# Kernel optimization log

Measured on AMD Instinct MI355X. Metric: run time of the kernel, lower is better.

## Reference

```python
import jax, jax.numpy as jnp
import numpy as np


def sh_enc_deg4(d):
    # d: [N,3] in [0,1]; tcnn maps to [-1,1] then evaluates degree-4 real SH (16 coeffs)
    v = d * 2.0 - 1.0
    x, y, z = v[:, 0], v[:, 1], v[:, 2]
    xy, yz, xz = x * y, y * z, x * z
    x2, y2, z2 = x * x, y * y, z * z
    sh = jnp.stack([
        jnp.full_like(x, 0.28209479177387814),
        -0.48860251190291987 * y,
        0.48860251190291987 * z,
        -0.48860251190291987 * x,
        1.0925484305920792 * xy,
        -1.0925484305920792 * yz,
        0.94617469575755997 * z2 - 0.31539156525251999,
        -1.0925484305920792 * xz,
        0.54627421529603959 * (x2 - y2),
        0.59004358992664352 * y * (-3.0 * x2 + y2),
        2.8906114426405538 * xy * z,
        0.45704579946446572 * y * (1.0 - 5.0 * z2),
        0.3731763325901154 * z * (5.0 * z2 - 3.0),
        0.45704579946446572 * x * (1.0 - 5.0 * z2),
        1.4453057213202769 * z * (x2 - y2),
        0.59004358992664352 * x * (x2 - 3.0 * y2),
    ], axis=-1)  # [N,16]
    return sh


def setup_inputs() -> dict:
    key = jax.random.key(0)
    k1, k2, k3, k4 = jax.random.split(key, 4)
    N = 2_097_152
    x = jax.random.uniform(k1, (N, 19), dtype=jnp.float32)
    # bias-free FullyFusedMLP: 32 -> 64 -> 64 -> 3
    W1 = jax.random.normal(k2, (32, 64), dtype=jnp.float32) * (1.0 / np.sqrt(32))
    W2 = jax.random.normal(k3, (64, 64), dtype=jnp.float32) * (1.0 / np.sqrt(64))
    W3 = jax.random.normal(k4, (64, 3), dtype=jnp.float32) * (1.0 / np.sqrt(64))
    return {"x": x, "W1": W1, "W2": W2, "W3": W3}


def reference(x, W1, W2, W3):
    # Composite encoding: SH(deg 4) on first 3 dims, Identity on the other 16 -> 32 features
    enc = jnp.concatenate([sh_enc_deg4(x[:, :3]), x[:, 3:]], axis=-1)  # [N,32]
    h = jax.nn.relu(enc @ W1)   # [N,64]
    h = jax.nn.relu(h @ W2)     # [N,64]
    out = h @ W3                # [N,3], linear output
    return out
```

## Files before the change

### kernel.cpp

```cpp
#include <hip/hip_runtime.h>
#include <hip/hip_bf16.h>


typedef short short8 __attribute__((ext_vector_type(8)));
typedef short short4v __attribute__((ext_vector_type(4)));
typedef float f32x4 __attribute__((ext_vector_type(4)));

#define MFMA16(a, b, c) __builtin_amdgcn_mfma_f32_16x16x32_bf16((a), (b), (c), 0, 0, 0)

static __device__ __forceinline__ short f2bf(float f) {
  __hip_bfloat16 h = __float2bfloat16(f);
  return __builtin_bit_cast(short, h);
}

#define LDS_PAD 68

__global__ __launch_bounds__(256) void fused_color_mlp(
    const float* __restrict__ x, const float* __restrict__ W1,
    const float* __restrict__ W2, const float* __restrict__ W3,
    float* __restrict__ out, int N) {
  __shared__ short h1s[4][16][LDS_PAD];
  __shared__ short h2s[4][16][LDS_PAD];

  const int tid = threadIdx.x;
  const int wv = tid >> 6;
  const int lane = tid & 63;
  const int row = lane & 15;
  const int kg = lane >> 4;

  short8 w1b[4];
#pragma unroll
  for (int cb = 0; cb < 4; ++cb) {
    short8 t;
#pragma unroll
    for (int j = 0; j < 8; ++j) t[j] = f2bf(W1[(kg * 8 + j) * 64 + cb * 16 + row]);
    w1b[cb] = t;
  }
  short8 w2b[2][4];
#pragma unroll
  for (int s = 0; s < 2; ++s)
#pragma unroll
    for (int cb = 0; cb < 4; ++cb) {
      short8 t;
#pragma unroll
      for (int j = 0; j < 8; ++j)
        t[j] = f2bf(W2[(s * 32 + kg * 8 + j) * 64 + cb * 16 + row]);
      w2b[s][cb] = t;
    }
  short8 w3b[2];
  const int c3r = (row < 3) ? row : 2;
#pragma unroll
  for (int s = 0; s < 2; ++s) {
    short8 t;
#pragma unroll
    for (int j = 0; j < 8; ++j) {
      short w = f2bf(W3[(s * 32 + kg * 8 + j) * 3 + c3r]);
      t[j] = (row < 3) ? w : (short)0;
    }
    w3b[s] = t;
  }

  const f32x4 zero = {0.f, 0.f, 0.f, 0.f};
  const long long gw = (long long)blockIdx.x * 4 + wv;
  const long long base = gw * 256;

  for (int it = 0; it < 16; ++it) {
    const long long p0 = base + (long long)it * 16;
    long long p = p0 + row;
    if (p > (long long)N - 1) p = (long long)N - 1;

    const float* xr = x + p * 19;
    const int off = (kg < 2) ? 0 : (3 + (kg - 2) * 8);
    float v[8];
#pragma unroll
    for (int j = 0; j < 8; ++j) v[j] = xr[off + j];

    float e[8];
    if (kg == 0) {
      float X = v[0] * 2.f - 1.f, Y = v[1] * 2.f - 1.f, Z = v[2] * 2.f - 1.f;
      e[0] = 0.28209479177387814f;
      e[1] = -0.48860251190291987f * Y;
      e[2] = 0.48860251190291987f * Z;
      e[3] = -0.48860251190291987f * X;
      e[4] = 1.0925484305920792f * X * Y;
      e[5] = -1.0925484305920792f * Y * Z;
      e[6] = 0.94617469575756f * Z * Z - 0.31539156525252f;
      e[7] = -1.0925484305920792f * X * Z;
    } else if (kg == 1) {
      float X = v[0] * 2.f - 1.f, Y = v[1] * 2.f - 1.f, Z = v[2] * 2.f - 1.f;
      float X2 = X * X, Y2 = Y * Y, Z2 = Z * Z;
      e[0] = 0.5462742152960396f * (X2 - Y2);
      e[1] = 0.5900435899266435f * Y * (-3.f * X2 + Y2);
      e[2] = 2.890611442640554f * X * Y * Z;
      e[3] = 0.4570457994644657f * Y * (1.f - 5.f * Z2);
      e[4] = 0.3731763325901154f * Z * (5.f * Z2 - 3.f);
      e[5] = 0.4570457994644657f * X * (1.f - 5.f * Z2);
      e[6] = 1.445305721320277f * Z * (X2 - Y2);
      e[7] = 0.5900435899266435f * X * (X2 - 3.f * Y2);
    } else {
#pragma unroll
      for (int j = 0; j < 8; ++j) e[j] = v[j];
    }
    short8 a0;
#pragma unroll
    for (int j = 0; j < 8; ++j) a0[j] = f2bf(e[j]);

    f32x4 c1[4];
#pragma unroll
    for (int cb = 0; cb < 4; ++cb) c1[cb] = MFMA16(a0, w1b[cb], zero);

#pragma unroll
    for (int cb = 0; cb < 4; ++cb)
#pragma unroll
      for (int r = 0; r < 4; ++r)
        h1s[wv][kg * 4 + r][cb * 16 + row] = f2bf(fmaxf(c1[cb][r], 0.f));
    __syncthreads();

    short8 a1[2];
#pragma unroll
    for (int s = 0; s < 2; ++s) {
      short4v lo = *(const short4v*)&h1s[wv][row][s * 32 + kg * 8];
      short4v hi = *(const short4v*)&h1s[wv][row][s * 32 + kg * 8 + 4];
      a1[s] = __builtin_shufflevector(lo, hi, 0, 1, 2, 3, 4, 5, 6, 7);
    }

    f32x4 c2[4];
#pragma unroll
    for (int cb = 0; cb < 4; ++cb) {
      f32x4 acc = MFMA16(a1[0], w2b[0][cb], zero);
      c2[cb] = MFMA16(a1[1], w2b[1][cb], acc);
    }

#pragma unroll
    for (int cb = 0; cb < 4; ++cb)
#pragma unroll
      for (int r = 0; r < 4; ++r)
        h2s[wv][kg * 4 + r][cb * 16 + row] = f2bf(fmaxf(c2[cb][r], 0.f));
    __syncthreads();

    short8 a2[2];
#pragma unroll
    for (int s = 0; s < 2; ++s) {
      short4v lo = *(const short4v*)&h2s[wv][row][s * 32 + kg * 8];
      short4v hi = *(const short4v*)&h2s[wv][row][s * 32 + kg * 8 + 4];
      a2[s] = __builtin_shufflevector(lo, hi, 0, 1, 2, 3, 4, 5, 6, 7);
    }

    f32x4 c3 = MFMA16(a2[0], w3b[0], zero);
    c3 = MFMA16(a2[1], w3b[1], c3);

    if (row < 3) {
#pragma unroll
      for (int r = 0; r < 4; ++r) {
        const long long q = p0 + kg * 4 + r;
        if (q < N) out[q * 3 + row] = c3[r];
      }
    }
  }
}

extern "C" void kernel_launch(void* const* d_in, const int* in_sizes, int n_in,
                              void* d_out, int out_size, void* d_ws, size_t ws_size,
                              hipStream_t stream) {
  (void)d_ws; (void)ws_size; (void)n_in; (void)out_size;
  const float* x = (const float*)d_in[0];
  const float* W1 = (const float*)d_in[1];
  const float* W2 = (const float*)d_in[2];
  const float* W3 = (const float*)d_in[3];
  float* out = (float*)d_out;
  const int N = in_sizes[0] / 19;
  const int blocks = (N + 1023) / 1024;
  fused_color_mlp<<<blocks, 256, 0, stream>>>(x, W1, W2, W3, out, N);
}
```

Baseline: 273.4 us.

## Move W3 fragments to LDS, raise occupancy bound, use 32-bit indexing

Stores the padded W3 bf16 fragments in shared memory and reloads them each iteration through an opaque pointer, so they no longer occupy registers for the whole kernel. Adds a min-blocks hint of 8 to launch_bounds so the compiler caps register use for higher occupancy. Replaces 64-bit index math with 32-bit ints to cut scalar and vector address work. The cost is extra LDS reads every iteration, one extra block barrier, and possible register spilling under the tighter bound.

```diff
diff --git a/kernel.cpp b/kernel.cpp
--- a/kernel.cpp
+++ b/kernel.cpp
@@ -14,19 +14,32 @@
 }
 
 #define LDS_PAD 68
+#define ITERS 16
 
-__global__ __launch_bounds__(256) void fused_color_mlp(
+__global__ __launch_bounds__(256, 8) void fused_color_mlp(
     const float* __restrict__ x, const float* __restrict__ W1,
     const float* __restrict__ W2, const float* __restrict__ W3,
     float* __restrict__ out, int N) {
   __shared__ short h1s[4][16][LDS_PAD];
   __shared__ short h2s[4][16][LDS_PAD];
+  __shared__ short w3f[64][16];
 
   const int tid = threadIdx.x;
   const int wv = tid >> 6;
   const int lane = tid & 63;
   const int row = lane & 15;
   const int kg = lane >> 4;
+
+  if (tid < 64) {
+    const int c3r = (row < 3) ? row : 2;
+#pragma unroll
+    for (int s = 0; s < 2; ++s)
+#pragma unroll
+      for (int j = 0; j < 8; ++j) {
+        short w = f2bf(W3[(s * 32 + kg * 8 + j) * 3 + c3r]);
+        w3f[lane][s * 8 + j] = (row < 3) ? w : (short)0;
+      }
+  }
 
   short8 w1b[4];
 #pragma unroll
@@ -47,27 +60,16 @@
         t[j] = f2bf(W2[(s * 32 + kg * 8 + j) * 64 + cb * 16 + row]);
       w2b[s][cb] = t;
     }
-  short8 w3b[2];
-  const int c3r = (row < 3) ? row : 2;
-#pragma unroll
-  for (int s = 0; s < 2; ++s) {
-    short8 t;
-#pragma unroll
-    for (int j = 0; j < 8; ++j) {
-      short w = f2bf(W3[(s * 32 + kg * 8 + j) * 3 + c3r]);
-      t[j] = (row < 3) ? w : (short)0;
-    }
-    w3b[s] = t;
-  }
+
+  __syncthreads();
 
   const f32x4 zero = {0.f, 0.f, 0.f, 0.f};
-  const long long gw = (long long)blockIdx.x * 4 + wv;
-  const long long base = gw * 256;
+  const int base = (blockIdx.x * 4 + wv) * (16 * ITERS / 16) * 16;
 
-  for (int it = 0; it < 16; ++it) {
-    const long long p0 = base + (long long)it * 16;
-    long long p = p0 + row;
-    if (p > (long long)N - 1) p = (long long)N - 1;
+  for (int it = 0; it < ITERS; ++it) {
+    const int p0 = base + it * 16;
+    int p = p0 + row;
+    if (p > N - 1) p = N - 1;
 
     const float* xr = x + p * 19;
     const int off = (kg < 2) ? 0 : (3 + (kg - 2) * 8);
@@ -146,13 +148,17 @@
       a2[s] = __builtin_shufflevector(lo, hi, 0, 1, 2, 3, 4, 5, 6, 7);
     }
 
-    f32x4 c3 = MFMA16(a2[0], w3b[0], zero);
-    c3 = MFMA16(a2[1], w3b[1], c3);
+    const short* wp = &w3f[lane][0];
+    asm("" : "+v"(wp));
+    short8 w3lo = *(const short8*)(wp);
+    short8 w3hi = *(const short8*)(wp + 8);
+    f32x4 c3 = MFMA16(a2[0], w3lo, zero);
+    c3 = MFMA16(a2[1], w3hi, c3);
 
     if (row < 3) {
 #pragma unroll
       for (int r = 0; r < 4; ++r) {
-        const long long q = p0 + kg * 4 + r;
+        const int q = p0 + kg * 4 + r;
         if (q < N) out[q * 3 + row] = c3[r];
       }
     }
@@ -169,6 +175,7 @@
   const float* W3 = (const float*)d_in[3];
   float* out = (float*)d_out;
   const int N = in_sizes[0] / 19;
-  const int blocks = (N + 1023) / 1024;
+  const int ppb = 4 * 16 * ITERS;
+  const int blocks = (N + ppb - 1) / ppb;
   fused_color_mlp<<<blocks, 256, 0, stream>>>(x, W1, W2, W3, out, N);
 }
```

New measurement: 376.5 us. 1.38x slower.
